# Optimization experiments

Hardware: AMD Instinct MI355X
Metric: run time of the kernel (lower is better)

## Reference

```python
import jax, jax.numpy as jnp
import numpy as np

N, E, DIM = 50000, 1_600_000, 96
H = DIM // 3      # num_heads = dim/3 = 32
HD = 3            # head_dim = dim/num_heads = 3
SCALE = 2.0
EPS = 1e-5


def ln(x, g, b):
    mu = x.mean(-1, keepdims=True)
    var = ((x - mu) ** 2).mean(-1, keepdims=True)
    return (x - mu) * jax.lax.rsqrt(var + EPS) * g + b


def setup_inputs() -> dict:
    key = jax.random.key(0)
    ks = jax.random.split(key, 40)
    rn = lambda k, shp, s=0.05: jax.random.normal(k, shp, jnp.float32) * s
    inp = {
        'feat': jax.random.normal(ks[0], (N, DIM), jnp.float32),
        'edge': jax.random.normal(ks[1], (E, H), jnp.float32),
        'Wq': rn(ks[2], (DIM, DIM)), 'bq': jnp.zeros((DIM,), jnp.float32),
        'Wk': rn(ks[3], (DIM, DIM)), 'bk': jnp.zeros((DIM,), jnp.float32),
        'Wv': rn(ks[4], (DIM, DIM)), 'bv': jnp.zeros((DIM,), jnp.float32),
        'We': rn(ks[5], (H, H)), 'be': jnp.zeros((H,), jnp.float32),
        'Wb': rn(ks[6], (H, H)), 'bb': jnp.zeros((H,), jnp.float32),
        'Wvv': rn(ks[7], (DIM + H, DIM)), 'bvv': jnp.zeros((DIM,), jnp.float32),
        'Wf0': rn(ks[8], (H, 2 * H)), 'bf0': jnp.zeros((2 * H,), jnp.float32),
        'Wf1': rn(ks[9], (2 * H, H)), 'bf1': jnp.zeros((H,), jnp.float32),
        'Wm0': rn(ks[10], (DIM, 2 * DIM)), 'bm0': jnp.zeros((2 * DIM,), jnp.float32),
        'Wm1': rn(ks[11], (2 * DIM, DIM)), 'bm1': jnp.zeros((DIM,), jnp.float32),
        'g_n0': jnp.ones((DIM,), jnp.float32), 'b_n0': jnp.zeros((DIM,), jnp.float32),
        'g_e0': jnp.ones((H,), jnp.float32), 'b_e0': jnp.zeros((H,), jnp.float32),
        'g_e1': jnp.ones((H,), jnp.float32), 'b_e1': jnp.zeros((H,), jnp.float32),
        'g_m': jnp.ones((DIM,), jnp.float32), 'b_m': jnp.zeros((DIM,), jnp.float32),
        'w': jnp.zeros((1,), jnp.float32),
        'src': jax.random.randint(ks[12], (E,), 0, N),
        'dst': jax.random.randint(ks[13], (E,), 0, N),
    }
    return inp


def reference(feat, edge, Wq, bq, Wk, bk, Wv, bv, We, be, Wb, bb, Wvv, bvv,
              Wf0, bf0, Wf1, bf1, Wm0, bm0, Wm1, bm1,
              g_n0, b_n0, g_e0, b_e0, g_e1, b_e1, g_m, b_m, w, src, dst):
    n = feat.shape[0]
    h0 = ln(feat, g_n0, b_n0)            # [N, DIM]
    ew = ln(edge, g_e0, b_e0)            # [E, H]
    q = (h0 @ Wq + bq).reshape(n, H, HD)
    k = (h0 @ Wk + bk).reshape(n, H, HD)
    v = (h0 @ Wv + bv).reshape(n, H, HD)
    ve = (ew @ We + be)[:, :, None]       # [E, H, 1]
    B = ew @ Wb + bb                      # [E, H]
    # src_dot_dst('k','q'): (k[src] * q[dst]).sum(-1)
    score = jnp.sum(k[src] * q[dst], axis=-1) / SCALE + B   # [E, H]
    e = score + edge                       # [E, H]
    se = jnp.concatenate([v[src], ve], axis=-1)              # [E, H, 4]
    # edge_softmax: softmax over incoming edges of each dst node, per head
    m = jax.ops.segment_max(score, dst, num_segments=n)      # [N, H]
    ex = jnp.exp(score - m[dst])
    den = jax.ops.segment_sum(ex, dst, num_segments=n)
    att = (ex / den[dst])[:, :, None]                        # [E, H, 1]
    agg = jax.ops.segment_sum(att * se, dst, num_segments=n) # [N, H, 4]
    h = feat * (1.0 + w) + (agg.reshape(n, -1) @ Wvv + bvv)  # [N, DIM]
    # up_expert Mlp (pre-LN residual)
    hn = ln(h, g_m, b_m)
    h = h + (jax.nn.relu(hn @ Wm0 + bm0) @ Wm1 + bm1)
    # edge FFN residual
    en = ln(e, g_e1, b_e1)
    e = e + (jax.nn.relu(en @ Wf0 + bf0) @ Wf1 + bf1)
    return h, e
```

## Files before the change

### kernel.cpp

```cpp
#include <hip/hip_runtime.h>
#include <cstdint>
#include <cstddef>


typedef short  s16x8 __attribute__((ext_vector_type(8)));
typedef short  s16x4 __attribute__((ext_vector_type(4)));
typedef float  f32x4 __attribute__((ext_vector_type(4)));

__device__ __forceinline__ unsigned short f2b(float x) {
    union { float f; unsigned u; } v; v.f = x;
    unsigned r = v.u + 0x7FFF + ((v.u >> 16) & 1);
    return (unsigned short)(r >> 16);
}
__device__ __forceinline__ float b2f(unsigned short u) {
    union { unsigned u; float f; } v; v.u = ((unsigned)u) << 16; return v.f;
}

template<int MULTI, int LNA, int A16, int RELU, int RES>
__global__ __launch_bounds__(256) void mgemm_kernel(
    const void* __restrict__ Av, int lda,
    const float* __restrict__ B0, const float* __restrict__ B1,
    const float* __restrict__ B2, int ldb,
    const float* __restrict__ bias0, const float* __restrict__ bias1,
    const float* __restrict__ bias2,
    const float* __restrict__ lng, const float* __restrict__ lnbv,
    const float* __restrict__ resid, const float* __restrict__ wptr,
    float* __restrict__ C, int ldc, unsigned short* __restrict__ C16,
    int M, int K)
{
    __shared__ unsigned short sAL[64 * 200];
    __shared__ unsigned short sB[96 * 40];

    const int tid = threadIdx.x;
    const int m0 = blockIdx.x * 64;
    const int y  = blockIdx.y;
    const float* B = MULTI ? (y == 0 ? B0 : (y == 1 ? B1 : B2)) : B0;
    const int nbB = MULTI ? 0 : y * 96;
    const int nbC = y * 96;
    const int w = tid >> 6, l = tid & 63, fr = l & 15, kg = l >> 4;
    const int KP = K + 8;

    if (LNA) {
        const float* Af = (const float*)Av;
        const int row = 16 * w + fr;
        const int grow = m0 + row;
        float x[24];
        if (grow < M) {
            #pragma unroll
            for (int t = 0; t < 6; t++)
                *(float4*)&x[t * 4] = *(const float4*)(Af + (size_t)grow * lda + 24 * kg + t * 4);
        } else {
            #pragma unroll
            for (int t = 0; t < 24; t++) x[t] = 0.f;
        }
        float s = 0.f;
        #pragma unroll
        for (int t = 0; t < 24; t++) s += x[t];
        s += __shfl_xor(s, 16, 64); s += __shfl_xor(s, 32, 64);
        float mu = s * (1.f / 96.f);
        float v2 = 0.f;
        #pragma unroll
        for (int t = 0; t < 24; t++) { float d = x[t] - mu; v2 += d * d; }
        v2 += __shfl_xor(v2, 16, 64); v2 += __shfl_xor(v2, 32, 64);
        float rs = rsqrtf(v2 * (1.f / 96.f) + 1e-5f);
        #pragma unroll
        for (int t3 = 0; t3 < 3; t3++) {
            s16x8 yv;
            #pragma unroll
            for (int u = 0; u < 8; u++) {
                int cidx = 24 * kg + t3 * 8 + u;
                yv[u] = (short)f2b((x[t3 * 8 + u] - mu) * rs * lng[cidx] + lnbv[cidx]);
            }
            *(s16x8*)&sAL[row * KP + 24 * kg + t3 * 8] = yv;
        }
    } else {
        const int nseg = K >> 3;
        for (int idx = tid; idx < 64 * nseg; idx += 256) {
            int row = idx / nseg, k8 = (idx - row * nseg) * 8;
            int grow = m0 + row;
            s16x8 a8 = (s16x8){0, 0, 0, 0, 0, 0, 0, 0};
            if (grow < M) {
                if (A16) {
                    a8 = *(const s16x8*)((const unsigned short*)Av + (size_t)grow * lda + k8);
                } else {
                    const float* Af = (const float*)Av;
                    float4 v0 = *(const float4*)(Af + (size_t)grow * lda + k8);
                    float4 v1 = *(const float4*)(Af + (size_t)grow * lda + k8 + 4);
                    a8[0] = (short)f2b(v0.x); a8[1] = (short)f2b(v0.y);
                    a8[2] = (short)f2b(v0.z); a8[3] = (short)f2b(v0.w);
                    a8[4] = (short)f2b(v1.x); a8[5] = (short)f2b(v1.y);
                    a8[6] = (short)f2b(v1.z); a8[7] = (short)f2b(v1.w);
                }
            }
            *(s16x8*)&sAL[row * KP + k8] = a8;
        }
    }

    f32x4 acc[6];
    #pragma unroll
    for (int i = 0; i < 6; i++) acc[i] = (f32x4){0.f, 0.f, 0.f, 0.f};

    for (int kc = 0; kc < K; kc += 32) {
        #pragma unroll
        for (int r = 0; r < 3; r++) {
            int idx = tid + 256 * r;
            int k = idx / 24, n4 = (idx - k * 24) * 4;
            float4 v = *(const float4*)(B + (size_t)(kc + k) * ldb + nbB + n4);
            sB[(n4 + 0) * 40 + k] = f2b(v.x);
            sB[(n4 + 1) * 40 + k] = f2b(v.y);
            sB[(n4 + 2) * 40 + k] = f2b(v.z);
            sB[(n4 + 3) * 40 + k] = f2b(v.w);
        }
        __syncthreads();
        {
            s16x8 a = *(s16x8*)&sAL[(16 * w + fr) * KP + kc + kg * 8];
            #pragma unroll
            for (int nt = 0; nt < 6; nt++) {
                s16x8 b = *(s16x8*)&sB[(16 * nt + fr) * 40 + kg * 8];
                acc[nt] = __builtin_amdgcn_mfma_f32_16x16x32_bf16(a, b, acc[nt], 0, 0, 0);
            }
        }
        __syncthreads();
    }

    float scale = 1.f;
    if (RES) scale = wptr ? (1.f + wptr[0]) : 1.f;
    const float* biasp = MULTI ? (y == 0 ? bias0 : (y == 1 ? bias1 : bias2)) : bias0;
    const int bbase = MULTI ? 0 : nbB;

    #pragma unroll
    for (int nt = 0; nt < 6; nt++) {
        int cl = nt * 16 + fr;
        float bv = biasp[bbase + cl];
        int gcol = nbC + cl;
        #pragma unroll
        for (int r = 0; r < 4; r++) {
            int row = m0 + 16 * w + 4 * kg + r;
            if (row >= M) continue;
            float v = acc[nt][r] + bv;
            if (RELU) v = fmaxf(v, 0.f);
            if (RES) v += scale * resid[(size_t)row * ldc + gcol];
            C[(size_t)row * ldc + gcol] = v;
            if (MULTI && C16 != nullptr && y == 2)
                C16[(size_t)row * 96 + cl] = f2b(v);
        }
    }
}

__global__ __launch_bounds__(256) void count_kernel(
    const int* __restrict__ dst, int* __restrict__ cnt, int E)
{
    int i = blockIdx.x * 256 + threadIdx.x;
    if (i < E) atomicAdd(&cnt[dst[i]], 1);
}

__global__ __launch_bounds__(1024) void scan_kernel(
    const int* __restrict__ cnt, int* __restrict__ off, int* __restrict__ cur, int N)
{
    __shared__ int s[1024];
    const int tid = threadIdx.x;
    const int chunk = (N + 1023) >> 10;
    const int lo = tid * chunk;
    const int hi = min(lo + chunk, N);
    int sum = 0;
    for (int i = lo; i < hi; i++) sum += cnt[i];
    s[tid] = sum;
    __syncthreads();
    for (int d = 1; d < 1024; d <<= 1) {
        int v = (tid >= d) ? s[tid - d] : 0;
        __syncthreads();
        s[tid] += v;
        __syncthreads();
    }
    int base = (tid == 0) ? 0 : s[tid - 1];
    for (int i = lo; i < hi; i++) {
        off[i] = base; cur[i] = base;
        base += cnt[i];
    }
}

__global__ __launch_bounds__(256) void scatter_kernel(
    const int* __restrict__ dst, const int* __restrict__ src,
    int* __restrict__ cur, int* __restrict__ eidx,
    int* __restrict__ srcs, int* __restrict__ dsts, int E)
{
    int i = blockIdx.x * 256 + threadIdx.x;
    if (i < E) {
        int p = atomicAdd(&cur[dst[i]], 1);
        eidx[p] = i;
        srcs[p] = src[i];
        dsts[p] = dst[i];
    }
}

__global__ __launch_bounds__(256, 4) void edge_tile_kernel(
    const float* __restrict__ edge, const float* __restrict__ qkv,
    const int* __restrict__ eidx, const int* __restrict__ srcs,
    const int* __restrict__ dsts,
    const float* __restrict__ We, const float* __restrict__ be,
    const float* __restrict__ Wb, const float* __restrict__ bb,
    const float* __restrict__ Wf0, const float* __restrict__ bf0,
    const float* __restrict__ Wf1, const float* __restrict__ bf1,
    const float* __restrict__ ge0, const float* __restrict__ be0,
    const float* __restrict__ ge1, const float* __restrict__ be1,
    unsigned short* __restrict__ exve16, float* __restrict__ eout, int E)
{
    __shared__ float          sEV[64 * 36];
    __shared__ unsigned short sQK[64 * 44];
    __shared__ unsigned short sA [64 * 40];
    __shared__ unsigned short sB [64 * 40];
    __shared__ unsigned short sB2[32 * 72];
    __shared__ unsigned short sX [64 * 76];

    const int tid = threadIdx.x;
    const long long e0 = (long long)blockIdx.x * 64;
    const int w  = tid >> 6;
    const int l  = tid & 63;
    const int fr = l & 15;
    const int kg = l >> 4;

    {
        const int row = tid >> 2;
        const int j   = tid & 3;
        long long s = e0 + row;
        float q[24], k[24];
        if (s < E) {
            int dn = dsts[s], sn = srcs[s];
            const float* qp = qkv + (size_t)dn * 288 + 24 * j;
            const float* kp = qkv + (size_t)sn * 288 + 96 + 24 * j;
            #pragma unroll
            for (int t = 0; t < 6; t++) {
                *(float4*)&q[t * 4] = *(const float4*)(qp + t * 4);
                *(float4*)&k[t * 4] = *(const float4*)(kp + t * 4);
            }
        } else {
            #pragma unroll
            for (int t = 0; t < 24; t++) { q[t] = 0.f; k[t] = 0.f; }
        }
        s16x8 qkb;
        #pragma unroll
        for (int t = 0; t < 8; t++) {
            float d = k[3*t]*q[3*t] + k[3*t+1]*q[3*t+1] + k[3*t+2]*q[3*t+2];
            qkb[t] = (short)f2b(0.5f * d);
        }
        *(s16x8*)&sQK[row * 44 + 8 * j] = qkb;
    }

    #pragma unroll
    for (int rr = 0; rr < 2; rr++) {
        int idx = tid + 256 * rr;
        int row = idx >> 3, c4 = (idx & 7) * 4;
        long long s = e0 + row;
        float4 v = make_float4(0.f, 0.f, 0.f, 0.f);
        if (s < E) {
            int ge = eidx[s];
            v = *(const float4*)(edge + (size_t)ge * 32 + c4);
        }
        *(float4*)&sEV[row * 36 + c4] = v;
    }
    {
        int k = tid >> 3, c4 = (tid & 7) * 4;
        float4 vb = *(const float4*)(Wb + k * 32 + c4);
        float4 ve = *(const float4*)(We + k * 32 + c4);
        sB[(c4 + 0) * 40 + k] = f2b(vb.x); sB[(c4 + 1) * 40 + k] = f2b(vb.y);
        sB[(c4 + 2) * 40 + k] = f2b(vb.z); sB[(c4 + 3) * 40 + k] = f2b(vb.w);
        sB[(32 + c4 + 0) * 40 + k] = f2b(ve.x); sB[(32 + c4 + 1) * 40 + k] = f2b(ve.y);
        sB[(32 + c4 + 2) * 40 + k] = f2b(ve.z); sB[(32 + c4 + 3) * 40 + k] = f2b(ve.w);
    }
    #pragma unroll
    for (int rr = 0; rr < 2; rr++) {
        int idx = tid + 256 * rr;
        int k = idx >> 3, c4 = (idx & 7) * 4;
        float4 v = *(const float4*)(Wf1 + k * 32 + c4);
        sB2[(c4 + 0) * 72 + k] = f2b(v.x); sB2[(c4 + 1) * 72 + k] = f2b(v.y);
        sB2[(c4 + 2) * 72 + k] = f2b(v.z); sB2[(c4 + 3) * 72 + k] = f2b(v.w);
    }
    __syncthreads();

    {
        const int row = 16 * w + (tid & 15);
        const int q = (tid & 63) >> 4;
        float x[8];
        *(float4*)&x[0] = *(float4*)&sEV[row * 36 + 8 * q];
        *(float4*)&x[4] = *(float4*)&sEV[row * 36 + 8 * q + 4];
        float s = x[0] + x[1] + x[2] + x[3] + x[4] + x[5] + x[6] + x[7];
        s += __shfl_xor(s, 16, 64); s += __shfl_xor(s, 32, 64);
        float mu = s * (1.f / 32.f);
        float v2 = 0.f;
        #pragma unroll
        for (int i = 0; i < 8; i++) { float d = x[i] - mu; v2 += d * d; }
        v2 += __shfl_xor(v2, 16, 64); v2 += __shfl_xor(v2, 32, 64);
        float rs = rsqrtf(v2 * (1.f / 32.f) + 1e-5f);
        float4 g1 = *(const float4*)(ge0 + 8 * q), g2 = *(const float4*)(ge0 + 8 * q + 4);
        float4 b1 = *(const float4*)(be0 + 8 * q), b2 = *(const float4*)(be0 + 8 * q + 4);
        float gg[8] = {g1.x, g1.y, g1.z, g1.w, g2.x, g2.y, g2.z, g2.w};
        float bs[8] = {b1.x, b1.y, b1.z, b1.w, b2.x, b2.y, b2.z, b2.w};
        s16x8 y;
        #pragma unroll
        for (int i = 0; i < 8; i++)
            y[i] = (short)f2b((x[i] - mu) * rs * gg[i] + bs[i]);
        *(s16x8*)&sA[row * 40 + 8 * q] = y;
    }
    __syncthreads();

    f32x4 acc[4];
    {
        s16x8 a = *(s16x8*)&sA[(16 * w + fr) * 40 + kg * 8];
        #pragma unroll
        for (int nt = 0; nt < 4; nt++) {
            s16x8 b = *(s16x8*)&sB[(16 * nt + fr) * 40 + kg * 8];
            f32x4 z = {0.f, 0.f, 0.f, 0.f};
            acc[nt] = __builtin_amdgcn_mfma_f32_16x16x32_bf16(a, b, z, 0, 0, 0);
        }
    }
    __syncthreads();

    #pragma unroll
    for (int nt = 0; nt < 2; nt++) {
        int col = nt * 16 + fr;
        float bbv = bb[col];
        #pragma unroll
        for (int r = 0; r < 4; r++) {
            int row = 16 * w + 4 * kg + r;
            float sc = acc[nt][r] + b2f(sQK[row * 44 + col]) + bbv;
            sX[row * 76 + col] = f2b(__expf(sc));
            float er = sc + sEV[row * 36 + col];
            sEV[row * 36 + col] = er;
        }
    }
    #pragma unroll
    for (int nt = 2; nt < 4; nt++) {
        int col = (nt - 2) * 16 + fr;
        float bev = be[col];
        #pragma unroll
        for (int r = 0; r < 4; r++) {
            int row = 16 * w + 4 * kg + r;
            sX[row * 76 + 32 + col] = f2b(acc[nt][r] + bev);
        }
    }
    #pragma unroll
    for (int rr = 0; rr < 2; rr++) {
        int idx = tid + 256 * rr;
        int k = idx >> 4, c4 = (idx & 15) * 4;
        float4 v = *(const float4*)(Wf0 + k * 64 + c4);
        sB[(c4 + 0) * 40 + k] = f2b(v.x); sB[(c4 + 1) * 40 + k] = f2b(v.y);
        sB[(c4 + 2) * 40 + k] = f2b(v.z); sB[(c4 + 3) * 40 + k] = f2b(v.w);
    }
    __syncthreads();

    #pragma unroll
    for (int rr = 0; rr < 2; rr++) {
        int idx = tid + 256 * rr;
        int row = idx >> 3, c8 = (idx & 7) * 8;
        long long s = e0 + row;
        if (s < E)
            *(s16x8*)(exve16 + (size_t)s * 64 + c8) = *(s16x8*)&sX[row * 76 + c8];
    }
    {
        const int row = 16 * w + (tid & 15);
        const int q = (tid & 63) >> 4;
        float x[8];
        *(float4*)&x[0] = *(float4*)&sEV[row * 36 + 8 * q];
        *(float4*)&x[4] = *(float4*)&sEV[row * 36 + 8 * q + 4];
        float s = x[0] + x[1] + x[2] + x[3] + x[4] + x[5] + x[6] + x[7];
        s += __shfl_xor(s, 16, 64); s += __shfl_xor(s, 32, 64);
        float mu = s * (1.f / 32.f);
        float v2 = 0.f;
        #pragma unroll
        for (int i = 0; i < 8; i++) { float d = x[i] - mu; v2 += d * d; }
        v2 += __shfl_xor(v2, 16, 64); v2 += __shfl_xor(v2, 32, 64);
        float rs = rsqrtf(v2 * (1.f / 32.f) + 1e-5f);
        float4 g1 = *(const float4*)(ge1 + 8 * q), g2 = *(const float4*)(ge1 + 8 * q + 4);
        float4 b1 = *(const float4*)(be1 + 8 * q), b2 = *(const float4*)(be1 + 8 * q + 4);
        float gg[8] = {g1.x, g1.y, g1.z, g1.w, g2.x, g2.y, g2.z, g2.w};
        float bs[8] = {b1.x, b1.y, b1.z, b1.w, b2.x, b2.y, b2.z, b2.w};
        s16x8 y;
        #pragma unroll
        for (int i = 0; i < 8; i++)
            y[i] = (short)f2b((x[i] - mu) * rs * gg[i] + bs[i]);
        *(s16x8*)&sA[row * 40 + 8 * q] = y;
    }
    __syncthreads();

    {
        s16x8 a = *(s16x8*)&sA[(16 * w + fr) * 40 + kg * 8];
        #pragma unroll
        for (int nt = 0; nt < 4; nt++) {
            s16x8 b = *(s16x8*)&sB[(16 * nt + fr) * 40 + kg * 8];
            f32x4 z = {0.f, 0.f, 0.f, 0.f};
            f32x4 a2 = __builtin_amdgcn_mfma_f32_16x16x32_bf16(a, b, z, 0, 0, 0);
            int col = nt * 16 + fr;
            float b0v = bf0[col];
            #pragma unroll
            for (int r = 0; r < 4; r++) {
                int row = 16 * w + 4 * kg + r;
                sX[row * 76 + col] = f2b(fmaxf(a2[r] + b0v, 0.f));
            }
        }
    }
    __syncthreads();

    {
        s16x8 a0 = *(s16x8*)&sX[(16 * w + fr) * 76 + kg * 8];
        s16x8 a1 = *(s16x8*)&sX[(16 * w + fr) * 76 + 32 + kg * 8];
        #pragma unroll
        for (int nt = 0; nt < 2; nt++) {
            s16x8 b0 = *(s16x8*)&sB2[(16 * nt + fr) * 72 + kg * 8];
            s16x8 b1 = *(s16x8*)&sB2[(16 * nt + fr) * 72 + 32 + kg * 8];
            f32x4 z = {0.f, 0.f, 0.f, 0.f};
            f32x4 t = __builtin_amdgcn_mfma_f32_16x16x32_bf16(a0, b0, z, 0, 0, 0);
            t = __builtin_amdgcn_mfma_f32_16x16x32_bf16(a1, b1, t, 0, 0, 0);
            int col = nt * 16 + fr;
            float bf1v = bf1[col];
            #pragma unroll
            for (int r = 0; r < 4; r++) {
                int row = 16 * w + 4 * kg + r;
                float out = t[r] + sEV[row * 36 + col] + bf1v;
                sEV[row * 36 + col] = out;
            }
        }
    }
    __syncthreads();

    #pragma unroll
    for (int rr = 0; rr < 2; rr++) {
        int idx = tid + 256 * rr;
        int row = idx >> 3, c4 = (idx & 7) * 4;
        long long s = e0 + row;
        if (s < E) {
            int ge = eidx[s];
            *(float4*)(eout + (size_t)ge * 32 + c4) = *(float4*)&sEV[row * 36 + c4];
        }
    }
}

__global__ __launch_bounds__(256) void gather_kernel(
    const unsigned short* __restrict__ exve16, const unsigned short* __restrict__ v16,
    const int* __restrict__ srcs, const int* __restrict__ off,
    const int* __restrict__ cnt, unsigned short* __restrict__ agg16, int N)
{
    __shared__ unsigned short sV16[4][2][2][96];
    __shared__ unsigned short sE16[4][2][2][64];
    const int wave = threadIdx.x >> 6;
    const int lane = threadIdx.x & 63;
    const int head = lane & 31;
    const int half = lane >> 5;
    int n = blockIdx.x * 4 + wave;
    if (n >= N) return;
    const int o = off[n], d = cnt[n];
    float a0 = 0.f, a1 = 0.f, a2 = 0.f, a3 = 0.f, den = 0.f;
    for (int i = half; i < d; i += 4) {
        const int i2 = i + 2;
        {
            int sn = srcs[o + i];
            const unsigned short* vr = v16 + (size_t)sn * 96;
            const unsigned short* er = exve16 + (size_t)(o + i) * 64;
            if (head < 12)
                *(s16x8*)&sV16[wave][half][0][head * 8] = *(const s16x8*)(vr + head * 8);
            else if (head >= 24)
                *(s16x8*)&sE16[wave][half][0][(head - 24) * 8] = *(const s16x8*)(er + (head - 24) * 8);
        }
        if (i2 < d) {
            int sn = srcs[o + i2];
            const unsigned short* vr = v16 + (size_t)sn * 96;
            const unsigned short* er = exve16 + (size_t)(o + i2) * 64;
            if (head < 12)
                *(s16x8*)&sV16[wave][half][1][head * 8] = *(const s16x8*)(vr + head * 8);
            else if (head >= 24)
                *(s16x8*)&sE16[wave][half][1][(head - 24) * 8] = *(const s16x8*)(er + (head - 24) * 8);
        }
        __builtin_amdgcn_wave_barrier();
        {
            float ex = b2f(sE16[wave][half][0][head]);
            float vv = b2f(sE16[wave][half][0][32 + head]);
            a0 += ex * b2f(sV16[wave][half][0][head * 3]);
            a1 += ex * b2f(sV16[wave][half][0][head * 3 + 1]);
            a2 += ex * b2f(sV16[wave][half][0][head * 3 + 2]);
            a3 += ex * vv;
            den += ex;
        }
        if (i2 < d) {
            float ex = b2f(sE16[wave][half][1][head]);
            float vv = b2f(sE16[wave][half][1][32 + head]);
            a0 += ex * b2f(sV16[wave][half][1][head * 3]);
            a1 += ex * b2f(sV16[wave][half][1][head * 3 + 1]);
            a2 += ex * b2f(sV16[wave][half][1][head * 3 + 2]);
            a3 += ex * vv;
            den += ex;
        }
        __builtin_amdgcn_wave_barrier();
    }
    a0 += __shfl_xor(a0, 32, 64);
    a1 += __shfl_xor(a1, 32, 64);
    a2 += __shfl_xor(a2, 32, 64);
    a3 += __shfl_xor(a3, 32, 64);
    den += __shfl_xor(den, 32, 64);
    if (half == 0) {
        float sc = (d > 0) ? 1.f / den : 0.f;
        s16x4 ov;
        ov[0] = (short)f2b(a0 * sc);
        ov[1] = (short)f2b(a1 * sc);
        ov[2] = (short)f2b(a2 * sc);
        ov[3] = (short)f2b(a3 * sc);
        *(s16x4*)(agg16 + (size_t)n * 128 + head * 4) = ov;
    }
}

extern "C" void kernel_launch(void* const* d_in, const int* in_sizes, int n_in,
                              void* d_out, int out_size, void* d_ws, size_t ws_size,
                              hipStream_t stream)
{
    (void)n_in; (void)out_size; (void)ws_size;
    const float* feat = (const float*)d_in[0];
    const float* edge = (const float*)d_in[1];
    const float* Wq   = (const float*)d_in[2];
    const float* bq   = (const float*)d_in[3];
    const float* Wk   = (const float*)d_in[4];
    const float* bk   = (const float*)d_in[5];
    const float* Wv   = (const float*)d_in[6];
    const float* bv   = (const float*)d_in[7];
    const float* We   = (const float*)d_in[8];
    const float* be   = (const float*)d_in[9];
    const float* Wb   = (const float*)d_in[10];
    const float* bb   = (const float*)d_in[11];
    const float* Wvv  = (const float*)d_in[12];
    const float* bvv  = (const float*)d_in[13];
    const float* Wf0  = (const float*)d_in[14];
    const float* bf0  = (const float*)d_in[15];
    const float* Wf1  = (const float*)d_in[16];
    const float* bf1  = (const float*)d_in[17];
    const float* Wm0  = (const float*)d_in[18];
    const float* bm0  = (const float*)d_in[19];
    const float* Wm1  = (const float*)d_in[20];
    const float* bm1  = (const float*)d_in[21];
    const float* g_n0 = (const float*)d_in[22];
    const float* b_n0 = (const float*)d_in[23];
    const float* g_e0 = (const float*)d_in[24];
    const float* b_e0 = (const float*)d_in[25];
    const float* g_e1 = (const float*)d_in[26];
    const float* b_e1 = (const float*)d_in[27];
    const float* g_m  = (const float*)d_in[28];
    const float* b_m  = (const float*)d_in[29];
    const float* wsc  = (const float*)d_in[30];
    const int*   src  = (const int*)d_in[31];
    const int*   dst  = (const int*)d_in[32];

    const int N = in_sizes[0] / 96;
    const int E = in_sizes[1] / 32;

    float* ws    = (float*)d_ws;
    float* qkv   = ws;
    float* hp    = qkv + (size_t)N * 288;
    unsigned short* agg16 = (unsigned short*)(hp + (size_t)N * 96);
    unsigned short* v16   = agg16 + (size_t)N * 128;
    unsigned short* exve16 = v16 + (size_t)N * 96;
    int*   eidx  = (int*)(exve16 + (size_t)E * 64);
    int*   srcs  = eidx + E;
    int*   dsts  = srcs + E;
    int*   cnt   = dsts + E;
    int*   offv  = cnt + N;
    int*   cur   = offv + N;
    float* tbuf  = ws;
    float* hout  = (float*)d_out;
    float* eoutp = (float*)d_out + (size_t)N * 96;

    hipMemsetAsync(cnt, 0, (size_t)N * sizeof(int), stream);

    const int mt = (N + 63) / 64;
    const int et = (E + 255) / 256;

    count_kernel<<<et, 256, 0, stream>>>(dst, cnt, E);
    scan_kernel<<<1, 1024, 0, stream>>>(cnt, offv, cur, N);
    scatter_kernel<<<et, 256, 0, stream>>>(dst, src, cur, eidx, srcs, dsts, E);

    mgemm_kernel<1,1,0,0,0><<<dim3(mt, 3), 256, 0, stream>>>(
        feat, 96, Wq, Wk, Wv, 96, bq, bk, bv, g_n0, b_n0,
        nullptr, nullptr, qkv, 288, v16, N, 96);

    edge_tile_kernel<<<(E + 63) / 64, 256, 0, stream>>>(edge, qkv, eidx, srcs, dsts,
                                             We, be, Wb, bb, Wf0, bf0, Wf1, bf1,
                                             g_e0, b_e0, g_e1, b_e1,
                                             exve16, eoutp, E);

    gather_kernel<<<(N + 3) / 4, 256, 0, stream>>>(exve16, v16, srcs, offv, cnt, agg16, N);

    mgemm_kernel<0,0,1,0,1><<<dim3(mt, 1), 256, 0, stream>>>(
        agg16, 128, Wvv, Wvv, Wvv, 96, bvv, bvv, bvv, nullptr, nullptr,
        feat, wsc, hp, 96, nullptr, N, 128);
    mgemm_kernel<0,1,0,1,0><<<dim3(mt, 2), 256, 0, stream>>>(
        hp, 96, Wm0, Wm0, Wm0, 192, bm0, bm0, bm0, g_m, b_m,
        nullptr, nullptr, tbuf, 192, nullptr, N, 96);
    mgemm_kernel<0,0,0,0,1><<<dim3(mt, 1), 256, 0, stream>>>(
        tbuf, 192, Wm1, Wm1, Wm1, 96, bm1, bm1, bm1, nullptr, nullptr,
        hp, nullptr, hout, 96, nullptr, N, 192);
}
```

Baseline: 915.1 us.

## Store QKV as bf16 and build CSR positions from count-pass ranks

Measured after the change: 826.8 us. 1.11x faster.

```diff
diff --git a/kernel.cpp b/kernel.cpp
--- a/kernel.cpp
+++ b/kernel.cpp
@@ -139,23 +139,26 @@
             if (row >= M) continue;
             float v = acc[nt][r] + bv;
             if (RELU) v = fmaxf(v, 0.f);
-            if (RES) v += scale * resid[(size_t)row * ldc + gcol];
-            C[(size_t)row * ldc + gcol] = v;
-            if (MULTI && C16 != nullptr && y == 2)
-                C16[(size_t)row * 96 + cl] = f2b(v);
+            if (MULTI) {
+                C16[(size_t)row * 288 + gcol] = f2b(v);
+            } else {
+                if (RES) v += scale * resid[(size_t)row * ldc + gcol];
+                C[(size_t)row * ldc + gcol] = v;
+            }
         }
     }
 }
 
 __global__ __launch_bounds__(256) void count_kernel(
-    const int* __restrict__ dst, int* __restrict__ cnt, int E)
+    const int* __restrict__ dst, int* __restrict__ cnt,
+    int* __restrict__ rank, int E)
 {
     int i = blockIdx.x * 256 + threadIdx.x;
-    if (i < E) atomicAdd(&cnt[dst[i]], 1);
+    if (i < E) rank[i] = atomicAdd(&cnt[dst[i]], 1);
 }
 
 __global__ __launch_bounds__(1024) void scan_kernel(
-    const int* __restrict__ cnt, int* __restrict__ off, int* __restrict__ cur, int N)
+    const int* __restrict__ cnt, int* __restrict__ off, int N)
 {
     __shared__ int s[1024];
     const int tid = threadIdx.x;
@@ -174,19 +177,19 @@
     }
     int base = (tid == 0) ? 0 : s[tid - 1];
     for (int i = lo; i < hi; i++) {
-        off[i] = base; cur[i] = base;
+        off[i] = base;
         base += cnt[i];
     }
 }
 
 __global__ __launch_bounds__(256) void scatter_kernel(
     const int* __restrict__ dst, const int* __restrict__ src,
-    int* __restrict__ cur, int* __restrict__ eidx,
-    int* __restrict__ srcs, int* __restrict__ dsts, int E)
+    const int* __restrict__ off, const int* __restrict__ rank,
+    int* __restrict__ eidx, int* __restrict__ srcs, int* __restrict__ dsts, int E)
 {
     int i = blockIdx.x * 256 + threadIdx.x;
     if (i < E) {
-        int p = atomicAdd(&cur[dst[i]], 1);
+        int p = off[dst[i]] + rank[i];
         eidx[p] = i;
         srcs[p] = src[i];
         dsts[p] = dst[i];
@@ -194,7 +197,7 @@
 }
 
 __global__ __launch_bounds__(256, 4) void edge_tile_kernel(
-    const float* __restrict__ edge, const float* __restrict__ qkv,
+    const float* __restrict__ edge, const unsigned short* __restrict__ qkv16,
     const int* __restrict__ eidx, const int* __restrict__ srcs,
     const int* __restrict__ dsts,
     const float* __restrict__ We, const float* __restrict__ be,
@@ -223,24 +226,29 @@
         const int row = tid >> 2;
         const int j   = tid & 3;
         long long s = e0 + row;
-        float q[24], k[24];
+        float qv[24], kv[24];
         if (s < E) {
             int dn = dsts[s], sn = srcs[s];
-            const float* qp = qkv + (size_t)dn * 288 + 24 * j;
-            const float* kp = qkv + (size_t)sn * 288 + 96 + 24 * j;
-            #pragma unroll
-            for (int t = 0; t < 6; t++) {
-                *(float4*)&q[t * 4] = *(const float4*)(qp + t * 4);
-                *(float4*)&k[t * 4] = *(const float4*)(kp + t * 4);
+            const unsigned short* qp = qkv16 + (size_t)dn * 288 + 24 * j;
+            const unsigned short* kp = qkv16 + (size_t)sn * 288 + 96 + 24 * j;
+            #pragma unroll
+            for (int t = 0; t < 3; t++) {
+                s16x8 qa = *(const s16x8*)(qp + 8 * t);
+                s16x8 ka = *(const s16x8*)(kp + 8 * t);
+                #pragma unroll
+                for (int u = 0; u < 8; u++) {
+                    qv[8 * t + u] = b2f((unsigned short)qa[u]);
+                    kv[8 * t + u] = b2f((unsigned short)ka[u]);
+                }
             }
         } else {
             #pragma unroll
-            for (int t = 0; t < 24; t++) { q[t] = 0.f; k[t] = 0.f; }
+            for (int t = 0; t < 24; t++) { qv[t] = 0.f; kv[t] = 0.f; }
         }
         s16x8 qkb;
         #pragma unroll
         for (int t = 0; t < 8; t++) {
-            float d = k[3*t]*q[3*t] + k[3*t+1]*q[3*t+1] + k[3*t+2]*q[3*t+2];
+            float d = kv[3*t]*qv[3*t] + kv[3*t+1]*qv[3*t+1] + kv[3*t+2]*qv[3*t+2];
             qkb[t] = (short)f2b(0.5f * d);
         }
         *(s16x8*)&sQK[row * 44 + 8 * j] = qkb;
@@ -435,7 +443,7 @@
 }
 
 __global__ __launch_bounds__(256) void gather_kernel(
-    const unsigned short* __restrict__ exve16, const unsigned short* __restrict__ v16,
+    const unsigned short* __restrict__ exve16, const unsigned short* __restrict__ qkv16,
     const int* __restrict__ srcs, const int* __restrict__ off,
     const int* __restrict__ cnt, unsigned short* __restrict__ agg16, int N)
 {
@@ -453,7 +461,7 @@
         const int i2 = i + 2;
         {
             int sn = srcs[o + i];
-            const unsigned short* vr = v16 + (size_t)sn * 96;
+            const unsigned short* vr = qkv16 + (size_t)sn * 288 + 192;
             const unsigned short* er = exve16 + (size_t)(o + i) * 64;
             if (head < 12)
                 *(s16x8*)&sV16[wave][half][0][head * 8] = *(const s16x8*)(vr + head * 8);
@@ -462,7 +470,7 @@
         }
         if (i2 < d) {
             int sn = srcs[o + i2];
-            const unsigned short* vr = v16 + (size_t)sn * 96;
+            const unsigned short* vr = qkv16 + (size_t)sn * 288 + 192;
             const unsigned short* er = exve16 + (size_t)(o + i2) * 64;
             if (head < 12)
                 *(s16x8*)&sV16[wave][half][1][head * 8] = *(const s16x8*)(vr + head * 8);
@@ -549,18 +557,17 @@
     const int E = in_sizes[1] / 32;
 
     float* ws    = (float*)d_ws;
-    float* qkv   = ws;
-    float* hp    = qkv + (size_t)N * 288;
-    unsigned short* agg16 = (unsigned short*)(hp + (size_t)N * 96);
-    unsigned short* v16   = agg16 + (size_t)N * 128;
-    unsigned short* exve16 = v16 + (size_t)N * 96;
+    float* hp    = ws;
+    float* tbuf  = hp + (size_t)N * 96;
+    unsigned short* agg16 = (unsigned short*)(tbuf + (size_t)N * 192);
+    unsigned short* qkv16 = agg16 + (size_t)N * 128;
+    unsigned short* exve16 = qkv16 + (size_t)N * 288;
     int*   eidx  = (int*)(exve16 + (size_t)E * 64);
-    int*   srcs  = eidx + E;
+    int*   rank  = eidx + E;
+    int*   srcs  = rank + E;
     int*   dsts  = srcs + E;
     int*   cnt   = dsts + E;
     int*   offv  = cnt + N;
-    int*   cur   = offv + N;
-    float* tbuf  = ws;
     float* hout  = (float*)d_out;
     float* eoutp = (float*)d_out + (size_t)N * 96;
 
@@ -569,20 +576,20 @@
     const int mt = (N + 63) / 64;
     const int et = (E + 255) / 256;
 
-    count_kernel<<<et, 256, 0, stream>>>(dst, cnt, E);
-    scan_kernel<<<1, 1024, 0, stream>>>(cnt, offv, cur, N);
-    scatter_kernel<<<et, 256, 0, stream>>>(dst, src, cur, eidx, srcs, dsts, E);
+    count_kernel<<<et, 256, 0, stream>>>(dst, cnt, rank, E);
+    scan_kernel<<<1, 1024, 0, stream>>>(cnt, offv, N);
+    scatter_kernel<<<et, 256, 0, stream>>>(dst, src, offv, rank, eidx, srcs, dsts, E);
 
     mgemm_kernel<1,1,0,0,0><<<dim3(mt, 3), 256, 0, stream>>>(
         feat, 96, Wq, Wk, Wv, 96, bq, bk, bv, g_n0, b_n0,
-        nullptr, nullptr, qkv, 288, v16, N, 96);
-
-    edge_tile_kernel<<<(E + 63) / 64, 256, 0, stream>>>(edge, qkv, eidx, srcs, dsts,
+        nullptr, nullptr, nullptr, 0, qkv16, N, 96);
+
+    edge_tile_kernel<<<(E + 63) / 64, 256, 0, stream>>>(edge, qkv16, eidx, srcs, dsts,
                                              We, be, Wb, bb, Wf0, bf0, Wf1, bf1,
                                              g_e0, b_e0, g_e1, b_e1,
                                              exve16, eoutp, E);
 
-    gather_kernel<<<(N + 3) / 4, 256, 0, stream>>>(exve16, v16, srcs, offv, cnt, agg16, N);
+    gather_kernel<<<(N + 3) / 4, 256, 0, stream>>>(exve16, qkv16, srcs, offv, cnt, agg16, N);
 
     mgemm_kernel<0,0,1,0,1><<<dim3(mt, 1), 256, 0, stream>>>(
         agg16, 128, Wvv, Wvv, Wvv, 96, bvv, bvv, bvv, nullptr, nullptr,
```
